# Optimization experiments

Hardware: AMD Instinct MI355X
Metric: run time of the kernel (lower is better)

## Reference

```python
import math
import jax, jax.numpy as jnp
import numpy as np

B, T, E = 1, 4096, 768
H, D = 12, 64
RA_WINDOW = 512
INIT_GATES = (2.2, 0.6, 0.1)


def setup_inputs() -> dict:
    key = jax.random.key(0)
    ks = jax.random.split(key, 6)
    x = jax.random.normal(ks[0], (B, T, E), dtype=jnp.float32)
    # Linear weights stored as [in, out] (math-equivalent to torch's x @ W.T)
    s = 1.0 / math.sqrt(E)
    Wq = jax.random.normal(ks[1], (E, H * D), dtype=jnp.float32) * s
    Wk = jax.random.normal(ks[2], (E, H * D), dtype=jnp.float32) * s
    Wv = jax.random.normal(ks[3], (E, H * D), dtype=jnp.float32) * s
    Wo = jax.random.normal(ks[4], (H * D, E), dtype=jnp.float32) * s
    gates = jnp.tile(jnp.asarray(INIT_GATES, dtype=jnp.float32)[None, :], (H, 1))  # [H,3]
    u = jax.random.normal(ks[5], (H, D), dtype=jnp.float32) * 0.02
    return {"x": x, "Wq": Wq, "Wk": Wk, "Wv": Wv, "Wo": Wo, "gates": gates, "u": u}


def reference(x, Wq, Wk, Wv, Wo, gates, u):
    # projections -> [B,H,T,D]
    def proj(W):
        return (x @ W).reshape(B, T, H, D).transpose(0, 2, 1, 3)
    Q, K, V = proj(Wq), proj(Wk), proj(Wv)

    S = jnp.einsum('bhtd,bhsd->bhts', Q, K) / math.sqrt(D)  # [B,H,T,T]

    w = jax.nn.softmax(gates, axis=-1)  # [H,3]
    w_std = w[:, 0][None, :, None, None]
    w_rec = w[:, 1][None, :, None, None]
    w_disc = w[:, 2][None, :, None, None]

    logits = w_std * S + w_rec * jnp.swapaxes(S, -2, -1)

    # discoverability column bias from K via per-head u
    d_raw = jnp.einsum('bhtd,hd->bht', K, u)
    d = d_raw - jnp.mean(d_raw, axis=-1, keepdims=True)
    logits = logits + w_disc * d[:, :, None, :]

    # causal banded mask
    idx = jnp.arange(T)
    mask = (idx[None, :] <= idx[:, None]) & (jnp.abs(idx[None, :] - idx[:, None]) <= RA_WINDOW)
    logits = jnp.where(mask[None, None, :, :], logits, -jnp.inf)

    attn = jax.nn.softmax(logits, axis=-1)
    ctx = jnp.einsum('bhts,bhsd->bhtd', attn, V)
    out = ctx.transpose(0, 2, 1, 3).reshape(B, T, H * D) @ Wo
    return (out, attn)
```

## Files before the change

### kernel.cpp

```cpp
#include <hip/hip_runtime.h>
#include <cstddef>

#define T_LEN 4096
#define EMB 768
#define NH 12
#define HD 64
#define WIN 512

#define GBM 128
#define GBN 128
#define GBK 16

__global__ __launch_bounds__(256) void gemm3_f32(const float* __restrict__ A,
                                                 const float* __restrict__ B0,
                                                 const float* __restrict__ B1,
                                                 const float* __restrict__ B2,
                                                 float* __restrict__ C0,
                                                 float* __restrict__ C1,
                                                 float* __restrict__ C2,
                                                 int M, int N, int K) {
    __shared__ float As[GBK][GBM + 4];
    __shared__ float Bs[GBK][GBN + 4];
    const int tid = threadIdx.x;
    const int bm = blockIdx.y * GBM;
    const int bn = blockIdx.x * GBN;
    const float* __restrict__ B = (blockIdx.z == 0) ? B0 : (blockIdx.z == 1) ? B1 : B2;
    float* __restrict__ C = (blockIdx.z == 0) ? C0 : (blockIdx.z == 1) ? C1 : C2;

    const int ty = (tid >> 4) << 2;
    const int tx = (tid & 15) << 2;

    const int ar = tid >> 1;
    const int ac = (tid & 1) << 3;
    const int br = tid >> 4;
    const int bc = (tid & 15) << 3;

    float acc[8][8] = {};

    float4 pa0 = *(const float4*)&A[(size_t)(bm + ar) * K + ac];
    float4 pa1 = *(const float4*)&A[(size_t)(bm + ar) * K + ac + 4];
    float4 pb0 = *(const float4*)&B[(size_t)br * N + bn + bc];
    float4 pb1 = *(const float4*)&B[(size_t)br * N + bn + bc + 4];

    for (int k0 = 0; k0 < K; k0 += GBK) {
        As[ac + 0][ar] = pa0.x; As[ac + 1][ar] = pa0.y; As[ac + 2][ar] = pa0.z; As[ac + 3][ar] = pa0.w;
        As[ac + 4][ar] = pa1.x; As[ac + 5][ar] = pa1.y; As[ac + 6][ar] = pa1.z; As[ac + 7][ar] = pa1.w;
        *(float4*)&Bs[br][bc]     = pb0;
        *(float4*)&Bs[br][bc + 4] = pb1;
        __syncthreads();
        if (k0 + GBK < K) {
            pa0 = *(const float4*)&A[(size_t)(bm + ar) * K + k0 + GBK + ac];
            pa1 = *(const float4*)&A[(size_t)(bm + ar) * K + k0 + GBK + ac + 4];
            pb0 = *(const float4*)&B[(size_t)(k0 + GBK + br) * N + bn + bc];
            pb1 = *(const float4*)&B[(size_t)(k0 + GBK + br) * N + bn + bc + 4];
        }
#pragma unroll
        for (int k = 0; k < GBK; ++k) {
            const float4 a0v = *(const float4*)&As[k][ty];
            const float4 a1v = *(const float4*)&As[k][ty + 64];
            const float4 b0v = *(const float4*)&Bs[k][tx];
            const float4 b1v = *(const float4*)&Bs[k][tx + 64];
            const float av[8] = {a0v.x, a0v.y, a0v.z, a0v.w, a1v.x, a1v.y, a1v.z, a1v.w};
            const float bv[8] = {b0v.x, b0v.y, b0v.z, b0v.w, b1v.x, b1v.y, b1v.z, b1v.w};
#pragma unroll
            for (int i = 0; i < 8; ++i)
#pragma unroll
                for (int j = 0; j < 8; ++j)
                    acc[i][j] += av[i] * bv[j];
        }
        __syncthreads();
    }
#pragma unroll
    for (int i = 0; i < 8; ++i) {
        const int r = bm + ty + ((i < 4) ? i : (60 + i));
        *(float4*)&C[(size_t)r * N + bn + tx]      = make_float4(acc[i][0], acc[i][1], acc[i][2], acc[i][3]);
        *(float4*)&C[(size_t)r * N + bn + tx + 64] = make_float4(acc[i][4], acc[i][5], acc[i][6], acc[i][7]);
    }
}

__global__ __launch_bounds__(256) void dbias_kernel(const float* __restrict__ K,
                                                    const float* __restrict__ u,
                                                    float* __restrict__ d_bias) {
    const int h = blockIdx.x;
    const int tid = threadIdx.x;
    __shared__ __align__(16) float us[HD];
    __shared__ float dr[T_LEN];
    __shared__ float red[256];
    if (tid < HD) us[tid] = u[h * HD + tid];
    __syncthreads();
    const float4* u4 = (const float4*)us;
    float lsum = 0.f;
    for (int t = tid; t < T_LEN; t += 256) {
        const float4* Kp = (const float4*)&K[(size_t)t * EMB + h * HD];
        float acc = 0.f;
#pragma unroll
        for (int i = 0; i < HD / 4; ++i) {
            float4 k4 = Kp[i];
            float4 uu = u4[i];
            acc += k4.x * uu.x + k4.y * uu.y + k4.z * uu.z + k4.w * uu.w;
        }
        dr[t] = acc;
        lsum += acc;
    }
    red[tid] = lsum;
    __syncthreads();
    for (int off = 128; off > 0; off >>= 1) {
        if (tid < off) red[tid] += red[tid + off];
        __syncthreads();
    }
    const float mean = red[0] * (1.0f / (float)T_LEN);
    __syncthreads();
    for (int t = tid; t < T_LEN; t += 256) {
        d_bias[h * T_LEN + t] = dr[t] - mean;
    }
}

__global__ __launch_bounds__(256) void attn_band_kernel(const float* __restrict__ Q,
                                                        const float* __restrict__ K,
                                                        const float* __restrict__ V,
                                                        const float* __restrict__ d_bias,
                                                        const float* __restrict__ gates,
                                                        float* __restrict__ attn,
                                                        float* __restrict__ ctx) {
    const int t0  = blockIdx.x << 6;
    const int h   = blockIdx.y;
    const int tid = threadIdx.x;
    const int tm  = (tid >> 4) << 2;
    const int tn4 = (tid & 15) << 2;
    const int lm  = tid >> 2;
    const int lk  = (tid & 3) << 2;

    __shared__ __align__(16) float QT[64][68];
    __shared__ __align__(16) float KT[64][68];
    __shared__ __align__(16) float Cc[64][68];
    __shared__ __align__(16) float Qs[64][68];
    __shared__ float cm[9][64];
    __shared__ float rmf[64];
    __shared__ float idvf[64];

    const float g0 = gates[h * 3 + 0];
    const float g1 = gates[h * 3 + 1];
    const float g2 = gates[h * 3 + 2];
    const float gm = fmaxf(g0, fmaxf(g1, g2));
    const float e0 = __expf(g0 - gm), e1 = __expf(g1 - gm), e2 = __expf(g2 - gm);
    const float gi = 1.0f / (e0 + e1 + e2);
    const float w_std = e0 * gi * 0.125f;
    const float w_rec = e1 * gi * 0.125f;
    const float w_disc = e2 * gi;

    {
        const float* Qp = Q + (size_t)(t0 + lm) * EMB + h * HD + lk;
        const float* Kp = K + (size_t)(t0 + lm) * EMB + h * HD + lk;
#pragma unroll
        for (int it = 0; it < 4; ++it) {
            float4 a = *(const float4*)(Qp + 16 * it);
            QT[lk + 16 * it + 0][lm] = a.x;
            QT[lk + 16 * it + 1][lm] = a.y;
            QT[lk + 16 * it + 2][lm] = a.z;
            QT[lk + 16 * it + 3][lm] = a.w;
            float4 b = *(const float4*)(Kp + 16 * it);
            KT[lk + 16 * it + 0][lm] = b.x;
            KT[lk + 16 * it + 1][lm] = b.y;
            KT[lk + 16 * it + 2][lm] = b.z;
            KT[lk + 16 * it + 3][lm] = b.w;
        }
    }

    const int s_base = (t0 - WIN > 0) ? (t0 - WIN) : 0;
    const int nch = ((t0 + 64) - s_base) >> 6;

    float rm[4], rden[4], acc[4][4];
#pragma unroll
    for (int i = 0; i < 4; ++i) {
        rm[i] = -1e30f;
        rden[i] = 0.f;
#pragma unroll
        for (int j = 0; j < 4; ++j) acc[i][j] = 0.f;
    }

    float4 kr[4], qr[4], vcur[4], vnxt[4];
    {
        const float* Kp = K + (size_t)(s_base + lm) * EMB + h * HD + lk;
        const float* Qp = Q + (size_t)(s_base + lm) * EMB + h * HD + lk;
        const float* Vp = V + (size_t)(s_base + lm) * EMB + h * HD + lk;
#pragma unroll
        for (int it = 0; it < 4; ++it) {
            kr[it]   = *(const float4*)(Kp + 16 * it);
            qr[it]   = *(const float4*)(Qp + 16 * it);
            vcur[it] = *(const float4*)(Vp + 16 * it);
        }
    }

    for (int c = 0; c < nch; ++c) {
        const int s0 = s_base + (c << 6);
        __syncthreads();
#pragma unroll
        for (int it = 0; it < 4; ++it) {
            Cc[lk + 16 * it + 0][lm] = kr[it].x;
            Cc[lk + 16 * it + 1][lm] = kr[it].y;
            Cc[lk + 16 * it + 2][lm] = kr[it].z;
            Cc[lk + 16 * it + 3][lm] = kr[it].w;
            Qs[lk + 16 * it + 0][lm] = qr[it].x;
            Qs[lk + 16 * it + 1][lm] = qr[it].y;
            Qs[lk + 16 * it + 2][lm] = qr[it].z;
            Qs[lk + 16 * it + 3][lm] = qr[it].w;
        }
        __syncthreads();
        if (c + 1 < nch) {
            const int s1 = s0 + 64;
            const float* Kp = K + (size_t)(s1 + lm) * EMB + h * HD + lk;
            const float* Qp = Q + (size_t)(s1 + lm) * EMB + h * HD + lk;
            const float* Vp = V + (size_t)(s1 + lm) * EMB + h * HD + lk;
#pragma unroll
            for (int it = 0; it < 4; ++it) {
                kr[it]   = *(const float4*)(Kp + 16 * it);
                qr[it]   = *(const float4*)(Qp + 16 * it);
                vnxt[it] = *(const float4*)(Vp + 16 * it);
            }
        }

        float m1[4][4] = {};
        float m2[4][4] = {};
#pragma unroll 8
        for (int k = 0; k < 64; ++k) {
            const float4 aq = *(const float4*)&QT[k][tm];
            const float4 bk = *(const float4*)&Cc[k][tn4];
            const float4 ak = *(const float4*)&KT[k][tm];
            const float4 bq = *(const float4*)&Qs[k][tn4];
            m1[0][0] += aq.x * bk.x; m1[0][1] += aq.x * bk.y; m1[0][2] += aq.x * bk.z; m1[0][3] += aq.x * bk.w;
            m1[1][0] += aq.y * bk.x; m1[1][1] += aq.y * bk.y; m1[1][2] += aq.y * bk.z; m1[1][3] += aq.y * bk.w;
            m1[2][0] += aq.z * bk.x; m1[2][1] += aq.z * bk.y; m1[2][2] += aq.z * bk.z; m1[2][3] += aq.z * bk.w;
            m1[3][0] += aq.w * bk.x; m1[3][1] += aq.w * bk.y; m1[3][2] += aq.w * bk.z; m1[3][3] += aq.w * bk.w;
            m2[0][0] += ak.x * bq.x; m2[0][1] += ak.x * bq.y; m2[0][2] += ak.x * bq.z; m2[0][3] += ak.x * bq.w;
            m2[1][0] += ak.y * bq.x; m2[1][1] += ak.y * bq.y; m2[1][2] += ak.y * bq.z; m2[1][3] += ak.y * bq.w;
            m2[2][0] += ak.z * bq.x; m2[2][1] += ak.z * bq.y; m2[2][2] += ak.z * bq.z; m2[2][3] += ak.z * bq.w;
            m2[3][0] += ak.w * bq.x; m2[3][1] += ak.w * bq.y; m2[3][2] += ak.w * bq.z; m2[3][3] += ak.w * bq.w;
        }

        const float4 db = *(const float4*)&d_bias[h * T_LEN + s0 + tn4];
        float l[4][4];
#pragma unroll
        for (int i = 0; i < 4; ++i) {
            const int t = t0 + tm + i;
            const float dbv[4] = {db.x, db.y, db.z, db.w};
#pragma unroll
            for (int j = 0; j < 4; ++j) {
                const int s = s0 + tn4 + j;
                float lv = w_std * m1[i][j] + w_rec * m2[i][j] + w_disc * dbv[j];
                const bool valid = (s <= t) && (s >= t - WIN);
                l[i][j] = valid ? lv : -1e30f;
            }
        }
        float cmx[4];
#pragma unroll
        for (int i = 0; i < 4; ++i)
            cmx[i] = fmaxf(fmaxf(l[i][0], l[i][1]), fmaxf(l[i][2], l[i][3]));
#pragma unroll
        for (int off = 1; off < 16; off <<= 1) {
#pragma unroll
            for (int i = 0; i < 4; ++i) cmx[i] = fmaxf(cmx[i], __shfl_xor(cmx[i], off));
        }
        float cs[4];
#pragma unroll
        for (int i = 0; i < 4; ++i) {
            const float nm = fmaxf(rm[i], cmx[i]);
            const float f = __expf(rm[i] - nm);
            float s = 0.f;
#pragma unroll
            for (int j = 0; j < 4; ++j) {
                const float p = __expf(l[i][j] - nm);
                l[i][j] = p;
                s += p;
            }
            cs[i] = s;
            rm[i] = nm;
            rden[i] *= f;
#pragma unroll
            for (int j = 0; j < 4; ++j) acc[i][j] *= f;
            *(float4*)&attn[((size_t)(h * T_LEN + t0 + tm + i)) * T_LEN + s0 + tn4] =
                make_float4(l[i][0], l[i][1], l[i][2], l[i][3]);
            if ((tid & 15) == 0) cm[c][tm + i] = nm;
        }
#pragma unroll
        for (int off = 1; off < 16; off <<= 1) {
#pragma unroll
            for (int i = 0; i < 4; ++i) cs[i] += __shfl_xor(cs[i], off);
        }
#pragma unroll
        for (int i = 0; i < 4; ++i) rden[i] += cs[i];

        __syncthreads();
#pragma unroll
        for (int i = 0; i < 4; ++i)
#pragma unroll
            for (int j = 0; j < 4; ++j)
                Cc[tn4 + j][tm + i] = l[i][j];
#pragma unroll
        for (int it = 0; it < 4; ++it)
            *(float4*)&Qs[lm][lk + 16 * it] = vcur[it];
        __syncthreads();

#pragma unroll 16
        for (int k = 0; k < 64; ++k) {
            const float4 av = *(const float4*)&Cc[k][tm];
            const float4 bv = *(const float4*)&Qs[k][tn4];
            acc[0][0] += av.x * bv.x; acc[0][1] += av.x * bv.y; acc[0][2] += av.x * bv.z; acc[0][3] += av.x * bv.w;
            acc[1][0] += av.y * bv.x; acc[1][1] += av.y * bv.y; acc[1][2] += av.y * bv.z; acc[1][3] += av.y * bv.w;
            acc[2][0] += av.z * bv.x; acc[2][1] += av.z * bv.y; acc[2][2] += av.z * bv.z; acc[2][3] += av.z * bv.w;
            acc[3][0] += av.w * bv.x; acc[3][1] += av.w * bv.y; acc[3][2] += av.w * bv.z; acc[3][3] += av.w * bv.w;
        }
#pragma unroll
        for (int it = 0; it < 4; ++it) vcur[it] = vnxt[it];
    }

    float idv[4];
#pragma unroll
    for (int i = 0; i < 4; ++i) {
        idv[i] = 1.0f / rden[i];
        *(float4*)&ctx[(size_t)(t0 + tm + i) * EMB + h * HD + tn4] =
            make_float4(acc[i][0] * idv[i], acc[i][1] * idv[i], acc[i][2] * idv[i], acc[i][3] * idv[i]);
    }
    if ((tid & 15) == 0) {
#pragma unroll
        for (int i = 0; i < 4; ++i) {
            rmf[tm + i] = rm[i];
            idvf[tm + i] = idv[i];
        }
    }
    __syncthreads();
    for (int idx = tid; idx < (nch << 6); idx += 256) {
        const int c = idx >> 6, r = idx & 63;
        cm[c][r] = __expf(cm[c][r] - rmf[r]) * idvf[r];
    }
    __syncthreads();
    for (int c = 0; c < nch; ++c) {
        const int s0 = s_base + (c << 6);
#pragma unroll
        for (int i = 0; i < 4; ++i) {
            float* p = &attn[((size_t)(h * T_LEN + t0 + tm + i)) * T_LEN + s0 + tn4];
            const float f = cm[c][tm + i];
            const float4 v = *(const float4*)p;
            *(float4*)p = make_float4(v.x * f, v.y * f, v.z * f, v.w * f);
        }
    }
    const int s_end = s_base + (nch << 6);
    const int wv = tid >> 6, ln = tid & 63;
    const float4 z4 = make_float4(0.f, 0.f, 0.f, 0.f);
    for (int r = wv; r < 64; r += 4) {
        float* arow = attn + ((size_t)(h * T_LEN + t0 + r)) * T_LEN;
        for (int col = ln << 2; col < s_base; col += 256)
            *(float4*)&arow[col] = z4;
        for (int col = s_end + (ln << 2); col < T_LEN; col += 256)
            *(float4*)&arow[col] = z4;
    }
}

extern "C" void kernel_launch(void* const* d_in, const int* in_sizes, int n_in,
                              void* d_out, int out_size, void* d_ws, size_t ws_size,
                              hipStream_t stream) {
    const float* x     = (const float*)d_in[0];
    const float* Wq    = (const float*)d_in[1];
    const float* Wk    = (const float*)d_in[2];
    const float* Wv    = (const float*)d_in[3];
    const float* Wo    = (const float*)d_in[4];
    const float* gates = (const float*)d_in[5];
    const float* u     = (const float*)d_in[6];

    float* out  = (float*)d_out;
    float* attn = out + (size_t)T_LEN * EMB;

    float* ws = (float*)d_ws;
    float* Qb = ws;
    float* Kb = Qb + (size_t)T_LEN * EMB;
    float* Vb = Kb + (size_t)T_LEN * EMB;
    float* Cb = Vb + (size_t)T_LEN * EMB;
    float* Db = Cb + (size_t)T_LEN * EMB;

    gemm3_f32<<<dim3(EMB / GBN, T_LEN / GBM, 3), 256, 0, stream>>>(
        x, Wq, Wk, Wv, Qb, Kb, Vb, T_LEN, EMB, EMB);
    dbias_kernel<<<NH, 256, 0, stream>>>(Kb, u, Db);

    attn_band_kernel<<<dim3(T_LEN / 64, NH), 256, 0, stream>>>(Qb, Kb, Vb, Db, gates,
                                                               attn, Cb);

    gemm3_f32<<<dim3(EMB / GBN, T_LEN / GBM, 1), 256, 0, stream>>>(
        Cb, Wo, Wo, Wo, out, out, out, T_LEN, EMB, EMB);
}
```

Baseline: 1.499 ms.

## Process 128-column key chunks and stream V directly from global memory

The banded attention loop now handles 128 key columns per iteration instead of 64, with a fixed 5-chunk range anchored at t0-576 and clamping for negative rows. The two score GEMMs (QK^T and KQ^T) run sequentially through one shared buffer, which shrinks shared memory and halves the number of chunk iterations. V is read straight from global memory inside the PV loop rather than staged in LDS. This trades fewer barriers and larger tiles for extra uncoalesced-ish global V loads and some wasted work on masked columns.

After: 1.496 ms. About the same (-0.2%).

```diff
diff --git a/kernel.cpp b/kernel.cpp
--- a/kernel.cpp
+++ b/kernel.cpp
@@ -125,18 +125,21 @@
     const int t0  = blockIdx.x << 6;
     const int h   = blockIdx.y;
     const int tid = threadIdx.x;
+    const int cg  = tid & 15;
     const int tm  = (tid >> 4) << 2;
-    const int tn4 = (tid & 15) << 2;
-    const int lm  = tid >> 2;
-    const int lk  = (tid & 3) << 2;
+    const int tn4 = cg << 2;
+
+    const int lm = tid >> 2;
+    const int lk = (tid & 3) << 4;
+    const int sr = tid >> 1;
+    const int sc = (tid & 1) << 5;
 
     __shared__ __align__(16) float QT[64][68];
     __shared__ __align__(16) float KT[64][68];
-    __shared__ __align__(16) float Cc[64][68];
-    __shared__ __align__(16) float Qs[64][68];
-    __shared__ float cm[9][64];
-    __shared__ float rmf[64];
-    __shared__ float idvf[64];
+    __shared__ __align__(16) float Bc[64][136];
+    __shared__ float cmf[5][64];
+    __shared__ float rmf[64], idvf[64];
+    float* __restrict__ Bp = &Bc[0][0];
 
     const float g0 = gates[h * 3 + 0];
     const float g1 = gates[h * 3 + 1];
@@ -148,26 +151,34 @@
     const float w_rec = e1 * gi * 0.125f;
     const float w_disc = e2 * gi;
 
+    const int cp_start = (t0 >= 576) ? 0 : ((576 - t0) >> 7);
+    int s0 = t0 - 576 + (cp_start << 7);
+
+    float4 kr[8], qr[8];
+    {
+        int srow = s0 + sr; srow = srow < 0 ? 0 : srow;
+        const float* Kp = K + (size_t)srow * EMB + h * HD + sc;
+#pragma unroll
+        for (int c = 0; c < 8; ++c) kr[c] = *(const float4*)(Kp + 4 * c);
+    }
+
     {
         const float* Qp = Q + (size_t)(t0 + lm) * EMB + h * HD + lk;
         const float* Kp = K + (size_t)(t0 + lm) * EMB + h * HD + lk;
 #pragma unroll
         for (int it = 0; it < 4; ++it) {
-            float4 a = *(const float4*)(Qp + 16 * it);
-            QT[lk + 16 * it + 0][lm] = a.x;
-            QT[lk + 16 * it + 1][lm] = a.y;
-            QT[lk + 16 * it + 2][lm] = a.z;
-            QT[lk + 16 * it + 3][lm] = a.w;
-            float4 b = *(const float4*)(Kp + 16 * it);
-            KT[lk + 16 * it + 0][lm] = b.x;
-            KT[lk + 16 * it + 1][lm] = b.y;
-            KT[lk + 16 * it + 2][lm] = b.z;
-            KT[lk + 16 * it + 3][lm] = b.w;
-        }
-    }
-
-    const int s_base = (t0 - WIN > 0) ? (t0 - WIN) : 0;
-    const int nch = ((t0 + 64) - s_base) >> 6;
+            float4 a = *(const float4*)(Qp + 4 * it);
+            QT[lk + 4 * it + 0][lm] = a.x;
+            QT[lk + 4 * it + 1][lm] = a.y;
+            QT[lk + 4 * it + 2][lm] = a.z;
+            QT[lk + 4 * it + 3][lm] = a.w;
+            float4 b = *(const float4*)(Kp + 4 * it);
+            KT[lk + 4 * it + 0][lm] = b.x;
+            KT[lk + 4 * it + 1][lm] = b.y;
+            KT[lk + 4 * it + 2][lm] = b.z;
+            KT[lk + 4 * it + 3][lm] = b.w;
+        }
+    }
 
     float rm[4], rden[4], acc[4][4];
 #pragma unroll
@@ -178,139 +189,137 @@
         for (int j = 0; j < 4; ++j) acc[i][j] = 0.f;
     }
 
-    float4 kr[4], qr[4], vcur[4], vnxt[4];
-    {
-        const float* Kp = K + (size_t)(s_base + lm) * EMB + h * HD + lk;
-        const float* Qp = Q + (size_t)(s_base + lm) * EMB + h * HD + lk;
-        const float* Vp = V + (size_t)(s_base + lm) * EMB + h * HD + lk;
-#pragma unroll
-        for (int it = 0; it < 4; ++it) {
-            kr[it]   = *(const float4*)(Kp + 16 * it);
-            qr[it]   = *(const float4*)(Qp + 16 * it);
-            vcur[it] = *(const float4*)(Vp + 16 * it);
-        }
-    }
-
-    for (int c = 0; c < nch; ++c) {
-        const int s0 = s_base + (c << 6);
-        __syncthreads();
-#pragma unroll
-        for (int it = 0; it < 4; ++it) {
-            Cc[lk + 16 * it + 0][lm] = kr[it].x;
-            Cc[lk + 16 * it + 1][lm] = kr[it].y;
-            Cc[lk + 16 * it + 2][lm] = kr[it].z;
-            Cc[lk + 16 * it + 3][lm] = kr[it].w;
-            Qs[lk + 16 * it + 0][lm] = qr[it].x;
-            Qs[lk + 16 * it + 1][lm] = qr[it].y;
-            Qs[lk + 16 * it + 2][lm] = qr[it].z;
-            Qs[lk + 16 * it + 3][lm] = qr[it].w;
-        }
-        __syncthreads();
-        if (c + 1 < nch) {
-            const int s1 = s0 + 64;
-            const float* Kp = K + (size_t)(s1 + lm) * EMB + h * HD + lk;
-            const float* Qp = Q + (size_t)(s1 + lm) * EMB + h * HD + lk;
-            const float* Vp = V + (size_t)(s1 + lm) * EMB + h * HD + lk;
-#pragma unroll
-            for (int it = 0; it < 4; ++it) {
-                kr[it]   = *(const float4*)(Kp + 16 * it);
-                qr[it]   = *(const float4*)(Qp + 16 * it);
-                vnxt[it] = *(const float4*)(Vp + 16 * it);
-            }
-        }
-
-        float m1[4][4] = {};
-        float m2[4][4] = {};
+    for (int cp = cp_start; cp < 5; ++cp) {
+        __syncthreads();
+#pragma unroll
+        for (int c = 0; c < 8; ++c) {
+            Bc[sc + 4 * c + 0][sr] = kr[c].x;
+            Bc[sc + 4 * c + 1][sr] = kr[c].y;
+            Bc[sc + 4 * c + 2][sr] = kr[c].z;
+            Bc[sc + 4 * c + 3][sr] = kr[c].w;
+        }
+        __syncthreads();
+
+        {
+            int srow = s0 + sr; srow = srow < 0 ? 0 : srow;
+            const float* Qp = Q + (size_t)srow * EMB + h * HD + sc;
+#pragma unroll
+            for (int c = 0; c < 8; ++c) qr[c] = *(const float4*)(Qp + 4 * c);
+        }
+
+        float m1[4][8] = {};
 #pragma unroll 8
         for (int k = 0; k < 64; ++k) {
-            const float4 aq = *(const float4*)&QT[k][tm];
-            const float4 bk = *(const float4*)&Cc[k][tn4];
-            const float4 ak = *(const float4*)&KT[k][tm];
-            const float4 bq = *(const float4*)&Qs[k][tn4];
-            m1[0][0] += aq.x * bk.x; m1[0][1] += aq.x * bk.y; m1[0][2] += aq.x * bk.z; m1[0][3] += aq.x * bk.w;
-            m1[1][0] += aq.y * bk.x; m1[1][1] += aq.y * bk.y; m1[1][2] += aq.y * bk.z; m1[1][3] += aq.y * bk.w;
-            m1[2][0] += aq.z * bk.x; m1[2][1] += aq.z * bk.y; m1[2][2] += aq.z * bk.z; m1[2][3] += aq.z * bk.w;
-            m1[3][0] += aq.w * bk.x; m1[3][1] += aq.w * bk.y; m1[3][2] += aq.w * bk.z; m1[3][3] += aq.w * bk.w;
-            m2[0][0] += ak.x * bq.x; m2[0][1] += ak.x * bq.y; m2[0][2] += ak.x * bq.z; m2[0][3] += ak.x * bq.w;
-            m2[1][0] += ak.y * bq.x; m2[1][1] += ak.y * bq.y; m2[1][2] += ak.y * bq.z; m2[1][3] += ak.y * bq.w;
-            m2[2][0] += ak.z * bq.x; m2[2][1] += ak.z * bq.y; m2[2][2] += ak.z * bq.z; m2[2][3] += ak.z * bq.w;
-            m2[3][0] += ak.w * bq.x; m2[3][1] += ak.w * bq.y; m2[3][2] += ak.w * bq.z; m2[3][3] += ak.w * bq.w;
-        }
-
-        const float4 db = *(const float4*)&d_bias[h * T_LEN + s0 + tn4];
-        float l[4][4];
+            const float4 a4 = *(const float4*)&QT[k][tm];
+            const float4 b0 = *(const float4*)&Bc[k][tn4];
+            const float4 b1 = *(const float4*)&Bc[k][tn4 + 64];
+            const float av[4] = {a4.x, a4.y, a4.z, a4.w};
+            const float bv[8] = {b0.x, b0.y, b0.z, b0.w, b1.x, b1.y, b1.z, b1.w};
+#pragma unroll
+            for (int i = 0; i < 4; ++i)
+#pragma unroll
+                for (int j = 0; j < 8; ++j)
+                    m1[i][j] += av[i] * bv[j];
+        }
+        __syncthreads();
+
+#pragma unroll
+        for (int c = 0; c < 8; ++c) {
+            Bc[sc + 4 * c + 0][sr] = qr[c].x;
+            Bc[sc + 4 * c + 1][sr] = qr[c].y;
+            Bc[sc + 4 * c + 2][sr] = qr[c].z;
+            Bc[sc + 4 * c + 3][sr] = qr[c].w;
+        }
+        __syncthreads();
+
+        if (cp < 4) {
+            int srow = s0 + 128 + sr; srow = srow < 0 ? 0 : srow;
+            const float* Kp = K + (size_t)srow * EMB + h * HD + sc;
+#pragma unroll
+            for (int c = 0; c < 8; ++c) kr[c] = *(const float4*)(Kp + 4 * c);
+        }
+
+        float m2[4][8] = {};
+#pragma unroll 8
+        for (int k = 0; k < 64; ++k) {
+            const float4 a4 = *(const float4*)&KT[k][tm];
+            const float4 b0 = *(const float4*)&Bc[k][tn4];
+            const float4 b1 = *(const float4*)&Bc[k][tn4 + 64];
+            const float av[4] = {a4.x, a4.y, a4.z, a4.w};
+            const float bv[8] = {b0.x, b0.y, b0.z, b0.w, b1.x, b1.y, b1.z, b1.w};
+#pragma unroll
+            for (int i = 0; i < 4; ++i)
+#pragma unroll
+                for (int j = 0; j < 8; ++j)
+                    m2[i][j] += av[i] * bv[j];
+        }
+
+        const int i0 = s0 + tn4;
+        const int i0c = i0 < 0 ? 0 : i0;
+        const float4 db0 = *(const float4*)&d_bias[h * T_LEN + i0c];
+        const float4 db1 = *(const float4*)&d_bias[h * T_LEN + s0 + 64 + tn4];
+        const float dbv[8] = {db0.x, db0.y, db0.z, db0.w, db1.x, db1.y, db1.z, db1.w};
+        float l[4][8];
 #pragma unroll
         for (int i = 0; i < 4; ++i) {
             const int t = t0 + tm + i;
-            const float dbv[4] = {db.x, db.y, db.z, db.w};
-#pragma unroll
-            for (int j = 0; j < 4; ++j) {
-                const int s = s0 + tn4 + j;
-                float lv = w_std * m1[i][j] + w_rec * m2[i][j] + w_disc * dbv[j];
-                const bool valid = (s <= t) && (s >= t - WIN);
+#pragma unroll
+            for (int j = 0; j < 8; ++j) {
+                const int s = s0 + ((j < 4) ? (tn4 + j) : (tn4 + j + 60));
+                const float lv = w_std * m1[i][j] + w_rec * m2[i][j] + w_disc * dbv[j];
+                const bool valid = (s >= 0) && (s <= t) && (s >= t - WIN);
                 l[i][j] = valid ? lv : -1e30f;
             }
         }
-        float cmx[4];
-#pragma unroll
-        for (int i = 0; i < 4; ++i)
-            cmx[i] = fmaxf(fmaxf(l[i][0], l[i][1]), fmaxf(l[i][2], l[i][3]));
-#pragma unroll
-        for (int off = 1; off < 16; off <<= 1) {
-#pragma unroll
-            for (int i = 0; i < 4; ++i) cmx[i] = fmaxf(cmx[i], __shfl_xor(cmx[i], off));
-        }
-        float cs[4];
 #pragma unroll
         for (int i = 0; i < 4; ++i) {
-            const float nm = fmaxf(rm[i], cmx[i]);
+            float cmx = fmaxf(fmaxf(fmaxf(l[i][0], l[i][1]), fmaxf(l[i][2], l[i][3])),
+                              fmaxf(fmaxf(l[i][4], l[i][5]), fmaxf(l[i][6], l[i][7])));
+#pragma unroll
+            for (int off = 1; off < 16; off <<= 1) cmx = fmaxf(cmx, __shfl_xor(cmx, off));
+            const float nm = fmaxf(rm[i], cmx);
             const float f = __expf(rm[i] - nm);
-            float s = 0.f;
-#pragma unroll
-            for (int j = 0; j < 4; ++j) {
+            float cs = 0.f;
+#pragma unroll
+            for (int j = 0; j < 8; ++j) {
                 const float p = __expf(l[i][j] - nm);
                 l[i][j] = p;
-                s += p;
+                cs += p;
             }
-            cs[i] = s;
+#pragma unroll
+            for (int off = 1; off < 16; off <<= 1) cs += __shfl_xor(cs, off);
+            rden[i] = rden[i] * f + cs;
             rm[i] = nm;
-            rden[i] *= f;
 #pragma unroll
             for (int j = 0; j < 4; ++j) acc[i][j] *= f;
-            *(float4*)&attn[((size_t)(h * T_LEN + t0 + tm + i)) * T_LEN + s0 + tn4] =
-                make_float4(l[i][0], l[i][1], l[i][2], l[i][3]);
-            if ((tid & 15) == 0) cm[c][tm + i] = nm;
-        }
-#pragma unroll
-        for (int off = 1; off < 16; off <<= 1) {
-#pragma unroll
-            for (int i = 0; i < 4; ++i) cs[i] += __shfl_xor(cs[i], off);
-        }
-#pragma unroll
-        for (int i = 0; i < 4; ++i) rden[i] += cs[i];
-
-        __syncthreads();
-#pragma unroll
-        for (int i = 0; i < 4; ++i)
-#pragma unroll
-            for (int j = 0; j < 4; ++j)
-                Cc[tn4 + j][tm + i] = l[i][j];
-#pragma unroll
-        for (int it = 0; it < 4; ++it)
-            *(float4*)&Qs[lm][lk + 16 * it] = vcur[it];
-        __syncthreads();
-
-#pragma unroll 16
-        for (int k = 0; k < 64; ++k) {
-            const float4 av = *(const float4*)&Cc[k][tm];
-            const float4 bv = *(const float4*)&Qs[k][tn4];
+            if (cg == 0) cmf[cp][tm + i] = nm;
+            float* arow = &attn[((size_t)(h * T_LEN + t0 + tm + i)) * T_LEN];
+            if (s0 >= 0)
+                *(float4*)&arow[s0 + tn4] = make_float4(l[i][0], l[i][1], l[i][2], l[i][3]);
+            *(float4*)&arow[s0 + 64 + tn4] = make_float4(l[i][4], l[i][5], l[i][6], l[i][7]);
+        }
+        __syncthreads();
+
+#pragma unroll
+        for (int j = 0; j < 4; ++j) {
+            *(float4*)&Bp[(tn4 + j) * 68 + tm] =
+                make_float4(l[0][j], l[1][j], l[2][j], l[3][j]);
+            *(float4*)&Bp[(tn4 + j + 64) * 68 + tm] =
+                make_float4(l[0][j + 4], l[1][j + 4], l[2][j + 4], l[3][j + 4]);
+        }
+        __syncthreads();
+
+#pragma unroll 8
+        for (int k = 0; k < 128; ++k) {
+            const float4 av = *(const float4*)&Bp[k * 68 + tm];
+            int vrow = s0 + k; vrow = vrow < 0 ? 0 : vrow;
+            const float4 bv = *(const float4*)&V[(size_t)vrow * EMB + h * HD + tn4];
             acc[0][0] += av.x * bv.x; acc[0][1] += av.x * bv.y; acc[0][2] += av.x * bv.z; acc[0][3] += av.x * bv.w;
             acc[1][0] += av.y * bv.x; acc[1][1] += av.y * bv.y; acc[1][2] += av.y * bv.z; acc[1][3] += av.y * bv.w;
             acc[2][0] += av.z * bv.x; acc[2][1] += av.z * bv.y; acc[2][2] += av.z * bv.z; acc[2][3] += av.z * bv.w;
             acc[3][0] += av.w * bv.x; acc[3][1] += av.w * bv.y; acc[3][2] += av.w * bv.z; acc[3][3] += av.w * bv.w;
         }
-#pragma unroll
-        for (int it = 0; it < 4; ++it) vcur[it] = vnxt[it];
+        s0 += 128;
     }
 
     float idv[4];
@@ -320,7 +329,7 @@
         *(float4*)&ctx[(size_t)(t0 + tm + i) * EMB + h * HD + tn4] =
             make_float4(acc[i][0] * idv[i], acc[i][1] * idv[i], acc[i][2] * idv[i], acc[i][3] * idv[i]);
     }
-    if ((tid & 15) == 0) {
+    if (cg == 0) {
 #pragma unroll
         for (int i = 0; i < 4; ++i) {
             rmf[tm + i] = rm[i];
@@ -328,29 +337,36 @@
         }
     }
     __syncthreads();
-    for (int idx = tid; idx < (nch << 6); idx += 256) {
+    for (int idx = tid; idx < 320; idx += 256) {
         const int c = idx >> 6, r = idx & 63;
-        cm[c][r] = __expf(cm[c][r] - rmf[r]) * idvf[r];
+        if (c >= cp_start) cmf[c][r] = __expf(cmf[c][r] - rmf[r]) * idvf[r];
     }
     __syncthreads();
-    for (int c = 0; c < nch; ++c) {
-        const int s0 = s_base + (c << 6);
-#pragma unroll
-        for (int i = 0; i < 4; ++i) {
-            float* p = &attn[((size_t)(h * T_LEN + t0 + tm + i)) * T_LEN + s0 + tn4];
-            const float f = cm[c][tm + i];
-            const float4 v = *(const float4*)p;
-            *(float4*)p = make_float4(v.x * f, v.y * f, v.z * f, v.w * f);
-        }
-    }
-    const int s_end = s_base + (nch << 6);
+    int ss = t0 - 576 + (cp_start << 7);
+    for (int cp = cp_start; cp < 5; ++cp, ss += 128) {
+#pragma unroll
+        for (int half = 0; half < 2; ++half) {
+            const int cbase = ss + (half << 6);
+            if (cbase >= 0) {
+#pragma unroll
+                for (int i = 0; i < 4; ++i) {
+                    const float f = cmf[cp][tm + i];
+                    float* p = &attn[((size_t)(h * T_LEN + t0 + tm + i)) * T_LEN + cbase + tn4];
+                    const float4 v = *(const float4*)p;
+                    *(float4*)p = make_float4(v.x * f, v.y * f, v.z * f, v.w * f);
+                }
+            }
+        }
+    }
+    const int sl = t0 - 576 + (cp_start << 7);
+    const int stored_left = sl < 0 ? 0 : sl;
     const int wv = tid >> 6, ln = tid & 63;
     const float4 z4 = make_float4(0.f, 0.f, 0.f, 0.f);
     for (int r = wv; r < 64; r += 4) {
         float* arow = attn + ((size_t)(h * T_LEN + t0 + r)) * T_LEN;
-        for (int col = ln << 2; col < s_base; col += 256)
+        for (int col = ln << 2; col < stored_left; col += 256)
             *(float4*)&arow[col] = z4;
-        for (int col = s_end + (ln << 2); col < T_LEN; col += 256)
+        for (int col = t0 + 64 + (ln << 2); col < T_LEN; col += 256)
             *(float4*)&arow[col] = z4;
     }
 }
```
